# Kernel tuning notes

Measured on AMD Instinct MI355X. Metric: run time of the kernel, lower is better.

## Reference

```python
import jax, jax.numpy as jnp
import numpy as np

ALPHA = 0.2
NEG = -9e15


def gat_layer(h, adj, W, a):
    # h: [B,N,Fin], adj: [B,N,N], W: [Fin,Fout], a: [2*Fout,1]
    Wh = jnp.matmul(h, W)                       # [B,N,Fout]
    Fout = W.shape[1]
    a1 = a[:Fout, 0]                             # source part
    a2 = a[Fout:, 0]                             # target part
    # e_ij = LeakyReLU(a1.Wh_i + a2.Wh_j) -- avoids O(N^2*2F) concat
    e = jax.nn.leaky_relu(
        (Wh @ a1)[:, :, None] + (Wh @ a2)[:, None, :], negative_slope=ALPHA
    )                                            # [B,N,N]
    att = jax.nn.softmax(jnp.where(adj > 0, e, NEG), axis=2)
    return jnp.matmul(att, Wh)                  # [B,N,Fout]


def setup_inputs() -> dict:
    key = jax.random.key(0)
    ks = jax.random.split(key, 6)
    B, N, F_IN, F_HID, F_OUT, H = 16, 1024, 256, 64, 64, 4
    x = jax.random.normal(ks[0], (B, N, F_IN), dtype=jnp.float32)
    adj = jax.random.randint(ks[1], (B, N, N), 0, 2, dtype=jnp.int32)
    W_heads = jax.random.normal(ks[2], (H, F_IN, F_HID), dtype=jnp.float32) * 0.1
    a_heads = jax.random.normal(ks[3], (H, 2 * F_HID, 1), dtype=jnp.float32) * 0.1
    W_out = jax.random.normal(ks[4], (H * F_HID, F_OUT), dtype=jnp.float32) * 0.1
    a_out = jax.random.normal(ks[5], (2 * F_OUT, 1), dtype=jnp.float32) * 0.1
    return {"x": x, "adj": adj, "W_heads": W_heads, "a_heads": a_heads,
            "W_out": W_out, "a_out": a_out}


def reference(x, adj, W_heads, a_heads, W_out, a_out):
    # multi-head: vmap over heads -> [H,B,N,F_hid]
    heads = jax.vmap(lambda W, a: gat_layer(x, adj, W, a))(W_heads, a_heads)
    H, B, N, Fh = heads.shape
    h_cat = jnp.transpose(heads, (1, 2, 0, 3)).reshape(B, N, H * Fh)
    out = jax.nn.elu(gat_layer(h_cat, adj, W_out, a_out))  # [B,N,nclass]
    return jnp.mean(out, axis=1)                           # [B,nclass]
```

## Files before the change

### kernel.cpp

```cpp
#include <hip/hip_runtime.h>
#include <math.h>

#define BB 16
#define NN 1024
#define FH 64
#define NH 4
#define LOG2E 1.4426950408889634f

typedef __attribute__((ext_vector_type(8))) short short8;
typedef __attribute__((ext_vector_type(4))) float f32x4;
typedef unsigned long long u64;
typedef unsigned short ushort_t;

__device__ inline unsigned f2bf(float x) {
    unsigned u = __builtin_bit_cast(unsigned, x);
    u += 0x7fff + ((u >> 16) & 1);
    return u >> 16;
}

__global__ void pack_kernel(const int* __restrict__ adj, u64* __restrict__ bm,
                            const float* __restrict__ Whd, const float* __restrict__ Wo,
                            ushort_t* __restrict__ BT1, ushort_t* __restrict__ BT2) {
    const int row = blockIdx.x * 4 + (threadIdx.x >> 6);
    const int lane = threadIdx.x & 63;
    const int* __restrict__ ar = adj + (size_t)row * NN;
    #pragma unroll
    for (int g = 0; g < 16; ++g) {
        u64 m = __ballot(ar[g * 64 + lane] > 0);
        if (lane == 0) bm[row * 16 + g] = m;
    }
    const int col = blockIdx.x, k = threadIdx.x;
    if (col < 256)      BT1[col * 256 + k] = (ushort_t)f2bf(Whd[(col >> 6) * 16384 + k * 64 + (col & 63)]);
    else if (col < 320) BT2[(col - 256) * 256 + k] = (ushort_t)f2bf(Wo[k * 64 + (col - 256)]);
}

template <int A_BF16>
__global__ __launch_bounds__(256, 4) void gemm_fused(
    const void* __restrict__ Ap, const ushort_t* __restrict__ BT,
    const float* __restrict__ av, ushort_t* __restrict__ WhbT,
    float* __restrict__ s1, float* __restrict__ s2, const int S) {
    constexpr int K = 256;
    __shared__ __align__(16) short tbuf[64][72];
    const int tid = threadIdx.x;
    const int w = tid >> 6, l = tid & 63, lo = l & 15, kg = l >> 4;

    const int nx = gridDim.x;
    const int id = blockIdx.y * nx + blockIdx.x;
    const int nwg = nx * gridDim.y;
    const int lid = (id & 7) * (nwg >> 3) + (id >> 3);
    const int row0 = (lid / nx) * 64, col0 = (lid % nx) * 64;

    const int b = row0 >> 10, j0 = row0 & (NN - 1);
    const int hsel = col0 >> 6;

    f32x4 acc[4];
    #pragma unroll
    for (int cb = 0; cb < 4; ++cb) acc[cb] = (f32x4){0.f, 0.f, 0.f, 0.f};

    if (A_BF16) {
        const ushort_t* __restrict__ arow = (const ushort_t*)Ap + (size_t)(row0 + w * 16 + lo) * K;
        #pragma unroll
        for (int ks = 0; ks < 8; ++ks) {
            const int k0 = ks * 32 + kg * 8;
            const short8 af = *(const short8*)(arow + k0);
            #pragma unroll
            for (int cb = 0; cb < 4; ++cb) {
                const short8 bf = *(const short8*)(BT + (size_t)(col0 + cb * 16 + lo) * K + k0);
                acc[cb] = __builtin_amdgcn_mfma_f32_16x16x32_bf16(af, bf, acc[cb], 0, 0, 0);
            }
        }
    } else {
        const float* __restrict__ arow = (const float*)Ap + (size_t)(row0 + w * 16 + lo) * K;
        #pragma unroll
        for (int ks = 0; ks < 8; ++ks) {
            const int k0 = ks * 32 + kg * 8;
            const float4 a0 = *(const float4*)(arow + k0);
            const float4 a1 = *(const float4*)(arow + k0 + 4);
            short8 af;
            af[0] = (short)f2bf(a0.x); af[1] = (short)f2bf(a0.y);
            af[2] = (short)f2bf(a0.z); af[3] = (short)f2bf(a0.w);
            af[4] = (short)f2bf(a1.x); af[5] = (short)f2bf(a1.y);
            af[6] = (short)f2bf(a1.z); af[7] = (short)f2bf(a1.w);
            #pragma unroll
            for (int cb = 0; cb < 4; ++cb) {
                const short8 bf = *(const short8*)(BT + (size_t)(col0 + cb * 16 + lo) * K + k0);
                acc[cb] = __builtin_amdgcn_mfma_f32_16x16x32_bf16(af, bf, acc[cb], 0, 0, 0);
            }
        }
    }

    float a1v[4], a2v[4];
    #pragma unroll
    for (int cb = 0; cb < 4; ++cb) {
        a1v[cb] = av[hsel * 128 + cb * 16 + lo];
        a2v[cb] = av[hsel * 128 + 64 + cb * 16 + lo];
    }
    float sp1[4], sp2[4];
    #pragma unroll
    for (int r = 0; r < 4; ++r) {
        sp1[r] = acc[0][r] * a1v[0] + acc[1][r] * a1v[1] + acc[2][r] * a1v[2] + acc[3][r] * a1v[3];
        sp2[r] = acc[0][r] * a2v[0] + acc[1][r] * a2v[1] + acc[2][r] * a2v[2] + acc[3][r] * a2v[3];
    }
    #pragma unroll
    for (int m = 1; m < 16; m <<= 1) {
        #pragma unroll
        for (int r = 0; r < 4; ++r) {
            sp1[r] += __shfl_xor(sp1[r], m);
            sp2[r] += __shfl_xor(sp2[r], m);
        }
    }
    if (lo == 0) {
        #pragma unroll
        for (int r = 0; r < 4; ++r) {
            const int R = row0 + w * 16 + kg * 4 + r;
            s1[hsel * (BB * NN) + R] = sp1[r];
            s2[hsel * (BB * NN) + R] = sp2[r];
        }
    }

    #pragma unroll
    for (int cb = 0; cb < 4; ++cb)
        #pragma unroll
        for (int rp = 0; rp < 2; ++rp) {
            unsigned lobf = f2bf(acc[cb][rp * 2]);
            unsigned hibf = f2bf(acc[cb][rp * 2 + 1]);
            ((unsigned*)tbuf)[(cb * 16 + lo) * 36 + w * 8 + kg * 2 + rp] = lobf | (hibf << 16);
        }
    __syncthreads();
    const int fl = tid >> 2, ch = tid & 3;
    const short8 v0 = *(const short8*)((const short*)tbuf + fl * 72 + ch * 16);
    const short8 v1 = *(const short8*)((const short*)tbuf + fl * 72 + ch * 16 + 8);
    ushort_t* dst = WhbT + ((size_t)(b * S) + col0 + fl) * NN + j0 + ch * 16;
    *(short8*)dst = v0;
    *(short8*)(dst + 8) = v1;
}

template <int H, int JQ, int OUT_BF16>
__global__ __launch_bounds__(256, 4) void apply_kernel(
    const ushort_t* __restrict__ WhbT, const int S,
    const float* __restrict__ s1, const float* __restrict__ s2,
    const unsigned* __restrict__ bm32,
    void* __restrict__ outp, float* __restrict__ sums) {
    constexpr int JLEN = NN / JQ;
    constexpr int BW = JLEN / 32;
    constexpr int NCH = JLEN / 64;
    constexpr int OB = OUT_BF16 ? (64 * 72 * 2) : (64 * 68 * 4);
    constexpr int SB = 2 * 8192;
    constexpr int UBUF = (SB > OB) ? SB : OB;

    __shared__ __align__(16) float s2s[JLEN];
    __shared__ unsigned bs[64][BW + 1];
    __shared__ __align__(16) char ubuf[UBUF];
    auto stage = (unsigned (*)[64][32])ubuf;

    const int Bk = blockIdx.x;
    const int lid = (Bk & 7) * 128 + (Bk >> 3);
    const int it = lid & 15;
    const int b  = (lid >> 4) & 15;
    const int z  = lid >> 8;
    const int h  = (H > 1) ? z : 0;
    const int jq = (JQ > 1) ? z : 0;
    const int j0g = jq * JLEN;

    const int tid = threadIdx.x;
    const int w = tid >> 6, l = tid & 63;
    const int lo = l & 15, kg = l >> 4;
    const int iloc = w * 16 + lo;
    const int rbase = b * NN + it * 64;
    const int gi = rbase + iloc;
    const int hb = h * (BB * NN);

    const ushort_t* __restrict__ whb = WhbT + ((size_t)(b * S + h * FH)) * NN + j0g;

    const int r0 = tid >> 3, st = tid & 7;
    const int sw = (st ^ (r0 & 7)) * 4;
    const size_t ga = (size_t)r0 * NN + st * 8;
    const size_t gb = (size_t)(r0 + 32) * NN + st * 8;

    int4 cva0 = *(const int4*)(whb + ga);
    int4 cva1 = *(const int4*)(whb + gb);

    const float* __restrict__ s2g = s2 + hb + b * NN + j0g;
    for (int k = tid; k < JLEN / 4; k += 256) {
        float4 v = *(const float4*)(s2g + k * 4);
        v.x *= LOG2E; v.y *= LOG2E; v.z *= LOG2E; v.w *= LOG2E;
        *(float4*)(s2s + k * 4) = v;
    }
    for (int idx = tid; idx < 64 * BW; idx += 256) {
        int r = idx / BW, wd = idx - r * BW;
        bs[r][wd] = bm32[(size_t)(rbase + r) * 32 + (j0g >> 5) + wd];
    }

    const float s1L = s1[hb + gi] * LOG2E;
    const float Arow = s1L;
    const float Brow = s1L * 0.2f;

    short8 ones;
    #pragma unroll
    for (int e = 0; e < 8; ++e) ones[e] = (short)0x3F80;

    f32x4 acc[4];
    #pragma unroll
    for (int fb = 0; fb < 4; ++fb) acc[fb] = (f32x4){0.f, 0.f, 0.f, 0.f};
    f32x4 accs = (f32x4){0.f, 0.f, 0.f, 0.f};

    *(int4*)&stage[0][r0][sw] = cva0;
    *(int4*)&stage[0][r0 + 32][sw] = cva1;
    if (1 < NCH) {
        cva0 = *(const int4*)(whb + 64 + ga);
        cva1 = *(const int4*)(whb + 64 + gb);
    }
    __syncthreads();

    #pragma unroll
    for (int c = 0; c < NCH; ++c) {
        int4 cvb0, cvb1;
        if (c + 2 < NCH) {
            const ushort_t* src = whb + (c + 2) * 64;
            cvb0 = *(const int4*)(src + ga);
            cvb1 = *(const int4*)(src + gb);
        }
        #pragma unroll
        for (int ks = 0; ks < 2; ++ks) {
            const int kb = c * 64 + ks * 32 + kg * 8;
            const unsigned byte = (bs[iloc][c * 2 + ks] >> (kg * 8)) & 0xFF;
            const float4 sa = *(const float4*)(s2s + kb);
            const float4 sb = *(const float4*)(s2s + kb + 4);
            const float s2r[8] = {sa.x, sa.y, sa.z, sa.w, sb.x, sb.y, sb.z, sb.w};
            short8 bfr;
            #pragma unroll
            for (int e = 0; e < 8; ++e) {
                const float t = s2r[e];
                const float u = Arow + t;
                const float v = __builtin_fmaf(t, 0.2f, Brow);
                float ev = fmaxf(u, v);
                ev = ((byte >> e) & 1) ? ev : -1.0e5f;
                bfr[e] = (short)f2bf(__builtin_amdgcn_exp2f(ev));
            }
            #pragma unroll
            for (int fb = 0; fb < 4; ++fb) {
                const int row = fb * 16 + lo;
                const int slot = (ks * 4 + kg) ^ (row & 7);
                const short8 afr = *(const short8*)&stage[c & 1][row][slot * 4];
                acc[fb] = __builtin_amdgcn_mfma_f32_16x16x32_bf16(afr, bfr, acc[fb], 0, 0, 0);
            }
            accs = __builtin_amdgcn_mfma_f32_16x16x32_bf16(ones, bfr, accs, 0, 0, 0);
        }
        if (c + 1 < NCH) {
            *(int4*)&stage[(c + 1) & 1][r0][sw] = cva0;
            *(int4*)&stage[(c + 1) & 1][r0 + 32][sw] = cva1;
        }
        cva0 = cvb0;
        cva1 = cvb1;
        __syncthreads();
    }

    if constexpr (OUT_BF16) {
        const float inv = 1.0f / accs[0];
        unsigned* ot = (unsigned*)ubuf;
        #pragma unroll
        for (int fb = 0; fb < 4; ++fb)
            #pragma unroll
            for (int rp = 0; rp < 2; ++rp) {
                unsigned lobf = f2bf(acc[fb][rp * 2] * inv);
                unsigned hibf = f2bf(acc[fb][rp * 2 + 1] * inv);
                ot[iloc * 36 + fb * 8 + kg * 2 + rp] = lobf | (hibf << 16);
            }
        __syncthreads();
        const int i2 = tid >> 2, ch = tid & 3;
        const short8 v0 = *(const short8*)((const short*)ubuf + i2 * 72 + ch * 16);
        const short8 v1 = *(const short8*)((const short*)ubuf + i2 * 72 + ch * 16 + 8);
        ushort_t* dst = (ushort_t*)outp + (size_t)(b * NN + it * 64 + i2) * 256 + h * FH + ch * 16;
        *(short8*)dst = v0;
        *(short8*)(dst + 8) = v1;
    } else {
        if (kg == 0) sums[(size_t)jq * (BB * NN) + rbase + iloc] = accs[0];
        float* ot = (float*)ubuf;
        #pragma unroll
        for (int fb = 0; fb < 4; ++fb)
            #pragma unroll
            for (int r = 0; r < 4; ++r)
                ot[iloc * 68 + fb * 16 + kg * 4 + r] = acc[fb][r];
        __syncthreads();
        const int i2 = tid >> 2, ch = tid & 3;
        float* dst = (float*)outp + (size_t)jq * (BB * NN * FH)
                   + (size_t)(b * NN + it * 64 + i2) * FH + ch * 16;
        *(f32x4*)dst        = *(const f32x4*)(ot + i2 * 68 + ch * 16);
        *(f32x4*)(dst + 4)  = *(const f32x4*)(ot + i2 * 68 + ch * 16 + 4);
        *(f32x4*)(dst + 8)  = *(const f32x4*)(ot + i2 * 68 + ch * 16 + 8);
        *(f32x4*)(dst + 12) = *(const f32x4*)(ot + i2 * 68 + ch * 16 + 12);
    }
}

__global__ __launch_bounds__(256) void mean1_kernel(const float* __restrict__ part,
                                                    const float* __restrict__ sums,
                                                    float* __restrict__ partial) {
    const int b = blockIdx.x, ck = blockIdx.y;
    const int tid = threadIdx.x;
    const int f = tid & 63, g = tid >> 6;
    float acc = 0.f;
    #pragma unroll
    for (int i = g; i < 64; i += 4) {
        const int row = b * NN + ck * 64 + i;
        const size_t base = (size_t)row * FH + f;
        const float srow = sums[row] + sums[row + 16384]
                         + sums[row + 32768] + sums[row + 49152];
        float v = part[base] + part[base + 1048576] + part[base + 2097152] + part[base + 3145728];
        v *= (1.0f / srow);
        v = (v > 0.f) ? v : (__builtin_amdgcn_exp2f(v * LOG2E) - 1.0f);
        acc += v;
    }
    __shared__ float r[4][64];
    r[g][f] = acc;
    __syncthreads();
    if (g == 0)
        partial[(b * 16 + ck) * FH + f] = r[0][f] + r[1][f] + r[2][f] + r[3][f];
}

__global__ __launch_bounds__(1024) void mean2_kernel(const float* __restrict__ partial,
                                                     float* __restrict__ out) {
    const int t = threadIdx.x;
    const int b = t >> 6, f = t & 63;
    float s = 0.f;
    #pragma unroll
    for (int ck = 0; ck < 16; ++ck) s += partial[(b * 16 + ck) * FH + f];
    out[b * FH + f] = s * (1.0f / NN);
}

extern "C" void kernel_launch(void* const* d_in, const int* in_sizes, int n_in,
                              void* d_out, int out_size, void* d_ws, size_t ws_size,
                              hipStream_t stream) {
    const float* x       = (const float*)d_in[0];
    const int*   adj     = (const int*)d_in[1];
    const float* W_heads = (const float*)d_in[2];
    const float* a_heads = (const float*)d_in[3];
    const float* W_out   = (const float*)d_in[4];
    const float* a_out   = (const float*)d_in[5];
    float* out = (float*)d_out;
    float* f0  = (float*)d_ws;

    ushort_t* hcat  = (ushort_t*)f0;
    ushort_t* WhbT1 = (ushort_t*)(f0 + 2097152);
    float*    part  = f0;
    ushort_t* WhbT2 = (ushort_t*)(f0 + 4194304);
    u64*      bmask = (u64*)(f0 + 4718592);
    ushort_t* WbT1  = (ushort_t*)(f0 + 5242880);
    ushort_t* WbT2  = (ushort_t*)(f0 + 5275648);
    float*    s1_1  = f0 + 5283840;
    float*    s2_1  = s1_1 + 65536;
    float*    s1_2  = s2_1 + 65536;
    float*    s2_2  = s1_2 + 16384;
    float*    sums2 = s2_2 + 16384;
    float*    partial = sums2 + 65536;

    dim3 blk(256);

    pack_kernel<<<dim3(BB * NN / 4), blk, 0, stream>>>(adj, bmask, W_heads, W_out, WbT1, WbT2);

    gemm_fused<0><<<dim3(4, 256), blk, 0, stream>>>(x, WbT1, a_heads, WhbT1, s1_1, s2_1, 256);
    apply_kernel<NH, 1, 1><<<dim3(1024), blk, 0, stream>>>(WhbT1, 256, s1_1, s2_1,
                                                           (const unsigned*)bmask, hcat, nullptr);

    gemm_fused<1><<<dim3(1, 256), blk, 0, stream>>>(hcat, WbT2, a_out, WhbT2, s1_2, s2_2, 64);
    apply_kernel<1, 4, 0><<<dim3(1024), blk, 0, stream>>>(WhbT2, 64, s1_2, s2_2,
                                                          (const unsigned*)bmask, part, sums2);

    mean1_kernel<<<dim3(BB, 16), blk, 0, stream>>>(part, sums2, partial);
    mean2_kernel<<<dim3(1), dim3(1024), 0, stream>>>(partial, out);
}
```

Measured before the change: 106.8 us.

## Use hardware bf16 packing, store partials in bf16, merge mean kernels, prioritize MFMA

Replaces the software float-to-bf16 rounding with the v_cvt_pk_bf16_f32 packed conversion in the GEMM and apply kernels. The LOG2E scaling of s2 moves into the GEMM epilogue, and the s_setprio calls raise wave priority around the MFMA block. Layer-2 partial outputs are now stored as bf16 instead of fp32, halving that traffic. The two mean kernels become one 16-block kernel, removing a launch but reducing parallelism and adding bf16 rounding error to the partial sums.

```diff
diff --git a/kernel.cpp b/kernel.cpp
--- a/kernel.cpp
+++ b/kernel.cpp
@@ -9,6 +9,7 @@
 
 typedef __attribute__((ext_vector_type(8))) short short8;
 typedef __attribute__((ext_vector_type(4))) float f32x4;
+typedef __attribute__((ext_vector_type(4))) unsigned u32x4;
 typedef unsigned long long u64;
 typedef unsigned short ushort_t;
 
@@ -16,6 +17,11 @@
     unsigned u = __builtin_bit_cast(unsigned, x);
     u += 0x7fff + ((u >> 16) & 1);
     return u >> 16;
+}
+__device__ inline unsigned pkbf(float lo, float hi) {
+    unsigned r;
+    asm("v_cvt_pk_bf16_f32 %0, %1, %2" : "=v"(r) : "v"(lo), "v"(hi));
+    return r;
 }
 
 __global__ void pack_kernel(const int* __restrict__ adj, u64* __restrict__ bm,
@@ -76,11 +82,10 @@
             const int k0 = ks * 32 + kg * 8;
             const float4 a0 = *(const float4*)(arow + k0);
             const float4 a1 = *(const float4*)(arow + k0 + 4);
-            short8 af;
-            af[0] = (short)f2bf(a0.x); af[1] = (short)f2bf(a0.y);
-            af[2] = (short)f2bf(a0.z); af[3] = (short)f2bf(a0.w);
-            af[4] = (short)f2bf(a1.x); af[5] = (short)f2bf(a1.y);
-            af[6] = (short)f2bf(a1.z); af[7] = (short)f2bf(a1.w);
+            u32x4 ap;
+            ap[0] = pkbf(a0.x, a0.y); ap[1] = pkbf(a0.z, a0.w);
+            ap[2] = pkbf(a1.x, a1.y); ap[3] = pkbf(a1.z, a1.w);
+            const short8 af = __builtin_bit_cast(short8, ap);
             #pragma unroll
             for (int cb = 0; cb < 4; ++cb) {
                 const short8 bf = *(const short8*)(BT + (size_t)(col0 + cb * 16 + lo) * K + k0);
@@ -114,18 +119,16 @@
         for (int r = 0; r < 4; ++r) {
             const int R = row0 + w * 16 + kg * 4 + r;
             s1[hsel * (BB * NN) + R] = sp1[r];
-            s2[hsel * (BB * NN) + R] = sp2[r];
+            s2[hsel * (BB * NN) + R] = sp2[r] * LOG2E;
         }
     }
 
     #pragma unroll
     for (int cb = 0; cb < 4; ++cb)
         #pragma unroll
-        for (int rp = 0; rp < 2; ++rp) {
-            unsigned lobf = f2bf(acc[cb][rp * 2]);
-            unsigned hibf = f2bf(acc[cb][rp * 2 + 1]);
-            ((unsigned*)tbuf)[(cb * 16 + lo) * 36 + w * 8 + kg * 2 + rp] = lobf | (hibf << 16);
-        }
+        for (int rp = 0; rp < 2; ++rp)
+            ((unsigned*)tbuf)[(cb * 16 + lo) * 36 + w * 8 + kg * 2 + rp] =
+                pkbf(acc[cb][rp * 2], acc[cb][rp * 2 + 1]);
     __syncthreads();
     const int fl = tid >> 2, ch = tid & 3;
     const short8 v0 = *(const short8*)((const short*)tbuf + fl * 72 + ch * 16);
@@ -144,9 +147,8 @@
     constexpr int JLEN = NN / JQ;
     constexpr int BW = JLEN / 32;
     constexpr int NCH = JLEN / 64;
-    constexpr int OB = OUT_BF16 ? (64 * 72 * 2) : (64 * 68 * 4);
     constexpr int SB = 2 * 8192;
-    constexpr int UBUF = (SB > OB) ? SB : OB;
+    constexpr int UBUF = SB;
 
     __shared__ __align__(16) float s2s[JLEN];
     __shared__ unsigned bs[64][BW + 1];
@@ -181,11 +183,8 @@
     int4 cva1 = *(const int4*)(whb + gb);
 
     const float* __restrict__ s2g = s2 + hb + b * NN + j0g;
-    for (int k = tid; k < JLEN / 4; k += 256) {
-        float4 v = *(const float4*)(s2g + k * 4);
-        v.x *= LOG2E; v.y *= LOG2E; v.z *= LOG2E; v.w *= LOG2E;
-        *(float4*)(s2s + k * 4) = v;
-    }
+    for (int k = tid; k < JLEN / 4; k += 256)
+        *(float4*)(s2s + k * 4) = *(const float4*)(s2g + k * 4);
     for (int idx = tid; idx < 64 * BW; idx += 256) {
         int r = idx / BW, wd = idx - r * BW;
         bs[r][wd] = bm32[(size_t)(rbase + r) * 32 + (j0g >> 5) + wd];
@@ -227,7 +226,7 @@
             const float4 sa = *(const float4*)(s2s + kb);
             const float4 sb = *(const float4*)(s2s + kb + 4);
             const float s2r[8] = {sa.x, sa.y, sa.z, sa.w, sb.x, sb.y, sb.z, sb.w};
-            short8 bfr;
+            float pv[8];
             #pragma unroll
             for (int e = 0; e < 8; ++e) {
                 const float t = s2r[e];
@@ -235,8 +234,13 @@
                 const float v = __builtin_fmaf(t, 0.2f, Brow);
                 float ev = fmaxf(u, v);
                 ev = ((byte >> e) & 1) ? ev : -1.0e5f;
-                bfr[e] = (short)f2bf(__builtin_amdgcn_exp2f(ev));
+                pv[e] = __builtin_amdgcn_exp2f(ev);
             }
+            u32x4 pk;
+            pk[0] = pkbf(pv[0], pv[1]); pk[1] = pkbf(pv[2], pv[3]);
+            pk[2] = pkbf(pv[4], pv[5]); pk[3] = pkbf(pv[6], pv[7]);
+            const short8 bfr = __builtin_bit_cast(short8, pk);
+            __builtin_amdgcn_s_setprio(1);
             #pragma unroll
             for (int fb = 0; fb < 4; ++fb) {
                 const int row = fb * 16 + lo;
@@ -245,6 +249,7 @@
                 acc[fb] = __builtin_amdgcn_mfma_f32_16x16x32_bf16(afr, bfr, acc[fb], 0, 0, 0);
             }
             accs = __builtin_amdgcn_mfma_f32_16x16x32_bf16(ones, bfr, accs, 0, 0, 0);
+            __builtin_amdgcn_s_setprio(0);
         }
         if (c + 1 < NCH) {
             *(int4*)&stage[(c + 1) & 1][r0][sw] = cva0;
@@ -255,76 +260,63 @@
         __syncthreads();
     }
 
+    const float inv = OUT_BF16 ? (1.0f / accs[0]) : 1.0f;
+    if (!OUT_BF16 && kg == 0)
+        sums[(size_t)jq * (BB * NN) + rbase + iloc] = accs[0];
+
+    unsigned* ot = (unsigned*)ubuf;
+    #pragma unroll
+    for (int fb = 0; fb < 4; ++fb)
+        #pragma unroll
+        for (int rp = 0; rp < 2; ++rp)
+            ot[iloc * 36 + fb * 8 + kg * 2 + rp] =
+                pkbf(acc[fb][rp * 2] * inv, acc[fb][rp * 2 + 1] * inv);
+    __syncthreads();
+    const int i2 = tid >> 2, ch = tid & 3;
+    const short8 v0 = *(const short8*)((const short*)ubuf + i2 * 72 + ch * 16);
+    const short8 v1 = *(const short8*)((const short*)ubuf + i2 * 72 + ch * 16 + 8);
     if constexpr (OUT_BF16) {
-        const float inv = 1.0f / accs[0];
-        unsigned* ot = (unsigned*)ubuf;
-        #pragma unroll
-        for (int fb = 0; fb < 4; ++fb)
-            #pragma unroll
-            for (int rp = 0; rp < 2; ++rp) {
-                unsigned lobf = f2bf(acc[fb][rp * 2] * inv);
-                unsigned hibf = f2bf(acc[fb][rp * 2 + 1] * inv);
-                ot[iloc * 36 + fb * 8 + kg * 2 + rp] = lobf | (hibf << 16);
-            }
-        __syncthreads();
-        const int i2 = tid >> 2, ch = tid & 3;
-        const short8 v0 = *(const short8*)((const short*)ubuf + i2 * 72 + ch * 16);
-        const short8 v1 = *(const short8*)((const short*)ubuf + i2 * 72 + ch * 16 + 8);
         ushort_t* dst = (ushort_t*)outp + (size_t)(b * NN + it * 64 + i2) * 256 + h * FH + ch * 16;
         *(short8*)dst = v0;
         *(short8*)(dst + 8) = v1;
     } else {
-        if (kg == 0) sums[(size_t)jq * (BB * NN) + rbase + iloc] = accs[0];
-        float* ot = (float*)ubuf;
-        #pragma unroll
-        for (int fb = 0; fb < 4; ++fb)
-            #pragma unroll
-            for (int r = 0; r < 4; ++r)
-                ot[iloc * 68 + fb * 16 + kg * 4 + r] = acc[fb][r];
-        __syncthreads();
-        const int i2 = tid >> 2, ch = tid & 3;
-        float* dst = (float*)outp + (size_t)jq * (BB * NN * FH)
-                   + (size_t)(b * NN + it * 64 + i2) * FH + ch * 16;
-        *(f32x4*)dst        = *(const f32x4*)(ot + i2 * 68 + ch * 16);
-        *(f32x4*)(dst + 4)  = *(const f32x4*)(ot + i2 * 68 + ch * 16 + 4);
-        *(f32x4*)(dst + 8)  = *(const f32x4*)(ot + i2 * 68 + ch * 16 + 8);
-        *(f32x4*)(dst + 12) = *(const f32x4*)(ot + i2 * 68 + ch * 16 + 12);
-    }
-}
-
-__global__ __launch_bounds__(256) void mean1_kernel(const float* __restrict__ part,
+        ushort_t* dst = (ushort_t*)outp + (size_t)jq * (BB * NN * FH)
+                      + (size_t)(b * NN + it * 64 + i2) * FH + ch * 16;
+        *(short8*)dst = v0;
+        *(short8*)(dst + 8) = v1;
+    }
+}
+
+__global__ __launch_bounds__(1024) void mean_kernel(const ushort_t* __restrict__ part,
                                                     const float* __restrict__ sums,
-                                                    float* __restrict__ partial) {
-    const int b = blockIdx.x, ck = blockIdx.y;
+                                                    float* __restrict__ out) {
+    const int b = blockIdx.x;
     const int tid = threadIdx.x;
     const int f = tid & 63, g = tid >> 6;
     float acc = 0.f;
-    #pragma unroll
-    for (int i = g; i < 64; i += 4) {
-        const int row = b * NN + ck * 64 + i;
-        const size_t base = (size_t)row * FH + f;
+    for (int i = g; i < NN; i += 16) {
+        const int row = b * NN + i;
         const float srow = sums[row] + sums[row + 16384]
                          + sums[row + 32768] + sums[row + 49152];
-        float v = part[base] + part[base + 1048576] + part[base + 2097152] + part[base + 3145728];
+        float v = 0.f;
+        #pragma unroll
+        for (int q = 0; q < 4; ++q) {
+            const unsigned u = part[(size_t)q * (BB * NN * FH) + (size_t)row * FH + f];
+            v += __builtin_bit_cast(float, u << 16);
+        }
         v *= (1.0f / srow);
         v = (v > 0.f) ? v : (__builtin_amdgcn_exp2f(v * LOG2E) - 1.0f);
         acc += v;
     }
-    __shared__ float r[4][64];
+    __shared__ float r[16][64];
     r[g][f] = acc;
     __syncthreads();
-    if (g == 0)
-        partial[(b * 16 + ck) * FH + f] = r[0][f] + r[1][f] + r[2][f] + r[3][f];
-}
-
-__global__ __launch_bounds__(1024) void mean2_kernel(const float* __restrict__ partial,
-                                                     float* __restrict__ out) {
-    const int t = threadIdx.x;
-    const int b = t >> 6, f = t & 63;
-    float s = 0.f;
-    #pragma unroll
-    for (int ck = 0; ck < 16; ++ck) s += partial[(b * 16 + ck) * FH + f];
-    out[b * FH + f] = s * (1.0f / NN);
+    if (g == 0) {
+        float s = 0.f;
+        #pragma unroll
+        for (int q = 0; q < 16; ++q) s += r[q][f];
+        out[b * FH + f] = s * (1.0f / NN);
+    }
 }
 
 extern "C" void kernel_launch(void* const* d_in, const int* in_sizes, int n_in,
@@ -340,8 +332,8 @@
     float* f0  = (float*)d_ws;
 
     ushort_t* hcat  = (ushort_t*)f0;
+    ushort_t* part  = (ushort_t*)f0;
     ushort_t* WhbT1 = (ushort_t*)(f0 + 2097152);
-    float*    part  = f0;
     ushort_t* WhbT2 = (ushort_t*)(f0 + 4194304);
     u64*      bmask = (u64*)(f0 + 4718592);
     ushort_t* WbT1  = (ushort_t*)(f0 + 5242880);
@@ -351,7 +343,6 @@
     float*    s1_2  = s2_1 + 65536;
     float*    s2_2  = s1_2 + 16384;
     float*    sums2 = s2_2 + 16384;
-    float*    partial = sums2 + 65536;
 
     dim3 blk(256);
 
@@ -365,6 +356,5 @@
     apply_kernel<1, 4, 0><<<dim3(1024), blk, 0, stream>>>(WhbT2, 64, s1_2, s2_2,
                                                           (const unsigned*)bmask, part, sums2);
 
-    mean1_kernel<<<dim3(BB, 16), blk, 0, stream>>>(part, sums2, partial);
-    mean2_kernel<<<dim3(1), dim3(1024), 0, stream>>>(partial, out);
-}
+    mean_kernel<<<dim3(BB), dim3(1024), 0, stream>>>(part, sums2, out);
+}
```

Result: slower. 130.1 us (+21.9%).
